# Optimization experiments

Hardware: AMD Instinct MI355X
Metric: run time of the kernel (lower is better)

Reference implementation:

```python
import jax, jax.numpy as jnp
import numpy as np


def _layernorm(x, g, b, eps=1e-5):
    m = jnp.mean(x, axis=-1, keepdims=True)
    v = jnp.var(x, axis=-1, keepdims=True)
    return (x - m) * jax.lax.rsqrt(v + eps) * g + b


def setup_inputs() -> dict:
    B, S, D, NS = 2, 1024, 1024, 2
    key = jax.random.key(0)
    ks = jax.random.split(key, 20)
    w = lambda k, shape: (jax.random.normal(k, shape, dtype=jnp.float32) * 0.02)
    return {
        "id_x": jax.random.normal(ks[0], (B, S, D), dtype=jnp.float32),
        "side": jax.random.normal(ks[1], (B, S, NS, D), dtype=jnp.float32),
        "num_heads": 16,
        "Wq": w(ks[2], (D, D)), "bq": jnp.zeros((D,), jnp.float32),
        "Wk": w(ks[3], (D, D)), "bk": jnp.zeros((D,), jnp.float32),
        "Wv": w(ks[4], (D, D)), "bv": jnp.zeros((D,), jnp.float32),
        "sWq": w(ks[5], (NS, D, D)), "sbq": jnp.zeros((NS, D), jnp.float32),
        "sWk": w(ks[6], (NS, D, D)), "sbk": jnp.zeros((NS, D), jnp.float32),
        "Wo": w(ks[7], (D, D)), "bo": jnp.zeros((D,), jnp.float32),
        "W1": w(ks[8], (D, D)), "b1": jnp.zeros((D,), jnp.float32),
        "W2": w(ks[9], (D, D)), "b2": jnp.zeros((D,), jnp.float32),
        "g1": jnp.ones((D,), jnp.float32), "be1": jnp.zeros((D,), jnp.float32),
        "g2": jnp.ones((D,), jnp.float32), "be2": jnp.zeros((D,), jnp.float32),
    }


def reference(id_x, side, num_heads, Wq, bq, Wk, bk, Wv, bv, sWq, sbq, sWk, sbk,
              Wo, bo, W1, b1, W2, b2, g1, be1, g2, be2):
    B, S, D = id_x.shape
    NS = side.shape[2]
    H = int(num_heads)
    dh = D // H
    scale = 1.0 / np.sqrt(D)  # source scales by sqrt(dim_H), not sqrt(head_dim)

    # id branch QKV: (B,S,H,dh)
    q = (id_x @ Wq + bq).reshape(B, S, H, dh)
    k = (id_x @ Wk + bk).reshape(B, S, H, dh)
    v = (id_x @ Wv + bv).reshape(B, S, H, dh)
    A_id = jax.nn.softmax(jnp.einsum('bqhd,bkhd->bhqk', q, k) * scale, axis=-1)

    # side branches: per-side Q/K projections, (B,S,NS,H,dh)
    sq = (jnp.einsum('bsnd,nde->bsne', side, sWq) + sbq).reshape(B, S, NS, H, dh)
    sk = (jnp.einsum('bsnd,nde->bsne', side, sWk) + sbk).reshape(B, S, NS, H, dh)
    A_side = jax.nn.softmax(
        jnp.einsum('bqnhd,bknhd->bnhqk', sq, sk) * scale, axis=-1)

    # fuse branches via elementwise max over (1+NS) attention maps
    A = jnp.max(jnp.concatenate([A_id[:, None], A_side], axis=1), axis=1)  # (B,H,q,k)

    O = jnp.einsum('bhqk,bkhd->bqhd', A, v).reshape(B, S, D)
    x = id_x + (O @ Wo + bo)          # residual + fc_o
    x = _layernorm(x, g1, be1)        # ln_mha (post-LN)

    # FF block with exact-erf gelu and residual
    h = jax.nn.gelu(x @ W1 + b1, approximate=False)
    x = x + (h @ W2 + b2)
    x = _layernorm(x, g2, be2)        # ln_ff
    return x
```

## Files before the change

### kernel.cpp

```cpp
#include <hip/hip_runtime.h>
#include <hip/hip_bf16.h>
#include <stdint.h>

typedef float   f32x4  __attribute__((ext_vector_type(4)));
typedef __bf16  bf16x8 __attribute__((ext_vector_type(8)));
typedef unsigned short u16x4 __attribute__((ext_vector_type(4)));
typedef unsigned short u16x8 __attribute__((ext_vector_type(8)));

__device__ __forceinline__ uint16_t f2b(float x) {
  union { float f; uint32_t u; } c; c.f = x;
  uint32_t u = c.u;
  return (uint16_t)((u + 0x7FFFu + ((u >> 16) & 1u)) >> 16);
}
__device__ __forceinline__ float b2f(uint16_t x) {
  union { uint32_t u; float f; } c; c.u = ((uint32_t)x) << 16;
  return c.f;
}

__device__ __forceinline__ f32x4 mfma32(bf16x8 a, bf16x8 b, f32x4 c) {
  return __builtin_amdgcn_mfma_f32_16x16x32_bf16(a, b, c, 0, 0, 0);
}

#define GLDS16(g, l) __builtin_amdgcn_global_load_lds( \
    (const __attribute__((address_space(1))) void*)(const void*)(g), \
    (__attribute__((address_space(3))) void*)(void*)(l), 16, 0, 0)

#define WAITVM(N) asm volatile("s_waitcnt vmcnt(" #N ")" ::: "memory")
#define WAITLGKM0 asm volatile("s_waitcnt lgkmcnt(0)" ::: "memory")
#define BAR() __builtin_amdgcn_s_barrier()

__global__ __launch_bounds__(256) void wtrans_all(
    const float* __restrict__ W0, const float* __restrict__ W1,
    const float* __restrict__ W2, const float* __restrict__ W3,
    const float* __restrict__ W4, const float* __restrict__ W5,
    const float* __restrict__ W6, const float* __restrict__ W7,
    const float* __restrict__ W8, const float* __restrict__ W9,
    uint16_t* __restrict__ WT,
    const float* __restrict__ bq, const float* __restrict__ bk,
    const float* __restrict__ bv, const float* __restrict__ sbq,
    const float* __restrict__ sbk, float* __restrict__ biasc,
    const float* __restrict__ id_x, const float* __restrict__ side,
    uint16_t* __restrict__ xb, uint16_t* __restrict__ sdb) {
  __shared__ float tl[32][33];
  const int tx = threadIdx.x, ty = threadIdx.y;
  if (blockIdx.z >= 11) {
    size_t zi = blockIdx.z - 11;
    size_t base = ((zi * 1024 + blockIdx.y * 32 + blockIdx.x) * 256
                   + ty * 32 + tx) * 4;
    const float* in; uint16_t* out;
    if (base < 2097152) { in = id_x; out = xb; }
    else { in = side; out = sdb; base -= 2097152; }
    f32x4 v = *(const f32x4*)(in + base);
    u16x4 o;
    o[0] = f2b(v[0]); o[1] = f2b(v[1]); o[2] = f2b(v[2]); o[3] = f2b(v[3]);
    *(u16x4*)(out + base) = o;
    return;
  }
  if (blockIdx.z == 10) {
    int i = (blockIdx.y * 32 + blockIdx.x) * 256 + ty * 32 + tx;
    if (i < 7168) {
      int seg = i >> 10, off = i & 1023;
      float v;
      switch (seg) {
        case 0: v = bq[off]; break;
        case 1: v = bk[off]; break;
        case 2: v = bv[off]; break;
        case 3: v = sbq[off]; break;
        case 4: v = sbk[off]; break;
        case 5: v = sbq[1024 + off]; break;
        default: v = sbk[1024 + off]; break;
      }
      biasc[i] = v;
    }
    return;
  }
  const float* W;
  switch (blockIdx.z) {
    case 0: W = W0; break; case 1: W = W1; break; case 2: W = W2; break;
    case 3: W = W3; break; case 4: W = W4; break; case 5: W = W5; break;
    case 6: W = W6; break; case 7: W = W7; break; case 8: W = W8; break;
    default: W = W9; break;
  }
  uint16_t* dst = WT + (size_t)blockIdx.z * 1048576;
  const int n0 = blockIdx.x * 32, k0 = blockIdx.y * 32;
#pragma unroll
  for (int i = 0; i < 32; i += 8)
    tl[ty + i][tx] = W[(size_t)(k0 + ty + i) * 1024 + n0 + tx];
  __syncthreads();
#pragma unroll
  for (int i = 0; i < 32; i += 8)
    dst[(size_t)(n0 + ty + i) * 1024 + k0 + tx] = f2b(tl[tx][ty + i]);
}

__global__ __launch_bounds__(512) void proj_k(
    const uint16_t* __restrict__ xb, const uint16_t* __restrict__ sdb,
    const uint16_t* __restrict__ WT, const float* __restrict__ biasc,
    uint16_t* __restrict__ qkv, uint16_t* __restrict__ sqk0,
    uint16_t* __restrict__ sqk1, uint16_t* __restrict__ vT) {
  __shared__ uint16_t As[2][8192];
  __shared__ uint16_t Bs[2][8192];
  const int xcd = blockIdx.x & 7, s = blockIdx.x >> 3;
  const uint16_t* A; const uint16_t* BT; const float* bias; uint16_t* C;
  int lda, ldc, bx, by;
  bool dovt = false;
  if (s < 48) {
    bx = xcd * 3 + s % 3; by = s / 3;
    A = xb; lda = 1024; BT = WT; bias = biasc; C = qkv; ldc = 3072;
    dovt = bx >= 16;
  } else if (s < 80) {
    int r = s - 48; bx = xcd * 2 + (r & 1); by = r >> 1;
    A = sdb; lda = 2048; BT = WT + 3145728; bias = biasc + 3072;
    C = sqk0; ldc = 2048;
  } else {
    int r = s - 80; bx = xcd * 2 + (r & 1); by = r >> 1;
    A = sdb + 1024; lda = 2048; BT = WT + 5242880; bias = biasc + 5120;
    C = sqk1; ldc = 2048;
  }
  const int t = threadIdx.x;
  const int lane = t & 63, w = t >> 6;
  const int wr = w >> 1, wc = w & 1;
  const int l15 = lane & 15, g = lane >> 4;
  const int bm0 = by * 128, bn0 = bx * 128;

  const int scol = ((t & 3) ^ ((t >> 3) & 3)) * 8;
  const uint16_t* ga = A  + (size_t)(bm0 + (t >> 2)) * lda  + scol;
  const uint16_t* gb = BT + (size_t)(bn0 + (t >> 2)) * 1024 + scol;
  const int gsw = (g ^ ((l15 >> 1) & 3)) * 8;

#define GSTAGE(bufi, k0) do { \
    GLDS16(ga + (k0),      &As[bufi][t * 8]); \
    GLDS16(ga + (k0) + 32, &As[bufi][4096 + t * 8]); \
    GLDS16(gb + (k0),      &Bs[bufi][t * 8]); \
    GLDS16(gb + (k0) + 32, &Bs[bufi][4096 + t * 8]); } while (0)

  f32x4 acc[2][4] = {};
  GSTAGE(0, 0);
  int cur = 0;
  for (int it = 0; it < 16; it++) {
    if (it < 15) { GSTAGE(cur ^ 1, (it + 1) * 64); WAITVM(4); }
    else WAITVM(0);
    BAR();
#pragma unroll
    for (int hf = 0; hf < 2; hf++) {
      const int ho = hf * 4096;
      bf16x8 af[2], bf[4];
#pragma unroll
      for (int i = 0; i < 2; i++)
        af[i] = *(const bf16x8*)&As[cur][ho + (wr * 32 + i * 16 + l15) * 32 + gsw];
#pragma unroll
      for (int i = 0; i < 4; i++)
        bf[i] = *(const bf16x8*)&Bs[cur][ho + (wc * 64 + i * 16 + l15) * 32 + gsw];
#pragma unroll
      for (int mi = 0; mi < 2; mi++)
#pragma unroll
        for (int ni = 0; ni < 4; ni++)
          acc[mi][ni] = mfma32(af[mi], bf[ni], acc[mi][ni]);
    }
    WAITLGKM0;
    BAR();
    cur ^= 1;
  }
#undef GSTAGE

#pragma unroll
  for (int mi = 0; mi < 2; mi++) {
#pragma unroll
    for (int ni = 0; ni < 4; ni++) {
      const int row0 = bm0 + wr * 32 + mi * 16 + g * 4;
      const int col  = bn0 + wc * 64 + ni * 16 + l15;
      const float bc = bias[col];
      u16x4 ov;
#pragma unroll
      for (int r = 0; r < 4; r++) {
        float v = acc[mi][ni][r] + bc;
        ov[r] = f2b(v);
        C[(size_t)(row0 + r) * ldc + col] = ov[r];
      }
      if (dovt) {
        const int cc = col - 2048, hh = cc >> 6, dd = cc & 63;
        const int bb = row0 >> 10, s0 = row0 & 1023;
        *(u16x4*)&vT[((size_t)((bb * 16 + hh) * 64 + dd)) * 1024 + s0] = ov;
      }
    }
  }
}

enum { EPI_BF16 = 0, EPI_RES = 1, EPI_GELU = 2 };

template<int EPI>
__global__ __launch_bounds__(256) void gemm64_k(
    const uint16_t* __restrict__ A, int lda,
    const uint16_t* __restrict__ BT,
    const float* __restrict__ bias,
    const float* __restrict__ res,
    void* __restrict__ Cv, int ldc) {
  __shared__ uint16_t As[4][4096];
  __shared__ uint16_t Bs[4][4096];
  const int t = threadIdx.x;
  const int lane = t & 63, w = t >> 6;
  const int wr = w >> 1, wc = w & 1;
  const int l15 = lane & 15, g = lane >> 4;
  const int bm0 = blockIdx.y * 64, bn0 = blockIdx.x * 64;

  const int scol = ((t & 3) ^ ((t >> 3) & 3)) * 8;
  const uint16_t* ga = A  + (size_t)(bm0 + (t >> 2)) * lda  + scol;
  const uint16_t* gb = BT + (size_t)(bn0 + (t >> 2)) * 1024 + scol;
  const int gsw = (g ^ ((l15 >> 1) & 3)) * 8;

#define GSTAGE64(bufi, k0) do { \
    GLDS16(ga + (k0),      &As[bufi][t * 8]); \
    GLDS16(ga + (k0) + 32, &As[bufi][2048 + t * 8]); \
    GLDS16(gb + (k0),      &Bs[bufi][t * 8]); \
    GLDS16(gb + (k0) + 32, &Bs[bufi][2048 + t * 8]); } while (0)

  f32x4 acc[2][2] = {};
  GSTAGE64(0, 0);
  GSTAGE64(1, 64);
  int cur = 0;
  for (int it = 0; it < 16; it++) {
    if (it < 14) {
      GSTAGE64((cur + 2) & 3, (it + 2) * 64);
      WAITVM(8);
    } else if (it == 14) {
      WAITVM(4);
    } else {
      WAITVM(0);
    }
    BAR();
#pragma unroll
    for (int hf = 0; hf < 2; hf++) {
      const int ho = hf * 2048;
      bf16x8 af[2], bf[2];
#pragma unroll
      for (int i = 0; i < 2; i++)
        af[i] = *(const bf16x8*)&As[cur][ho + (wr * 32 + i * 16 + l15) * 32 + gsw];
#pragma unroll
      for (int i = 0; i < 2; i++)
        bf[i] = *(const bf16x8*)&Bs[cur][ho + (wc * 32 + i * 16 + l15) * 32 + gsw];
#pragma unroll
      for (int mi = 0; mi < 2; mi++)
#pragma unroll
        for (int ni = 0; ni < 2; ni++)
          acc[mi][ni] = mfma32(af[mi], bf[ni], acc[mi][ni]);
    }
    cur = (cur + 1) & 3;
  }
#undef GSTAGE64

#pragma unroll
  for (int mi = 0; mi < 2; mi++) {
#pragma unroll
    for (int ni = 0; ni < 2; ni++) {
      const int row0 = bm0 + wr * 32 + mi * 16 + g * 4;
      const int col  = bn0 + wc * 32 + ni * 16 + l15;
      const float bc = bias[col];
#pragma unroll
      for (int r = 0; r < 4; r++) {
        float v = acc[mi][ni][r] + bc;
        const size_t idx = (size_t)(row0 + r) * ldc + col;
        if constexpr (EPI == EPI_RES) {
          ((float*)Cv)[idx] = v + res[idx];
        } else if constexpr (EPI == EPI_GELU) {
          float gl = 0.5f * v * (1.0f + erff(v * 0.70710678118654752f));
          ((uint16_t*)Cv)[idx] = f2b(gl);
        } else {
          ((uint16_t*)Cv)[idx] = f2b(v);
        }
      }
    }
  }
}

__global__ __launch_bounds__(256) void attn_z(
    const uint16_t* __restrict__ qkv,
    const uint16_t* __restrict__ sqk0,
    const uint16_t* __restrict__ sqk1,
    float* __restrict__ zp) {
  __shared__ uint16_t Ks0[3][2048];
  __shared__ uint16_t Ks1[3][2048];
  __shared__ uint16_t Ks2[3][2048];
  const int t = threadIdx.x;
  const int lane = t & 63, w = t >> 6;
  const int l15 = lane & 15, g = lane >> 4;
  const int bid = blockIdx.x;
  const int xcd = bid & 7, idx = bid >> 3;
  const int grp = xcd * 8 + (idx >> 4);
  const int qt = idx & 15;
  const int hb = grp >> 1, kc = grp & 1;
  const int b = hb >> 4, h = hb & 15;
  const int q0 = qt * 64 + w * 16;
  const float scl2 = 0.03125f * 1.44269504088896f;
  const size_t rq = (size_t)(b * 1024 + q0 + l15);

  bf16x8 qf[3][2];
  {
    const uint16_t* p = qkv + rq * 3072 + h * 64 + g * 8;
    qf[0][0] = *(const bf16x8*)p; qf[0][1] = *(const bf16x8*)(p + 32);
    p = sqk0 + rq * 2048 + h * 64 + g * 8;
    qf[1][0] = *(const bf16x8*)p; qf[1][1] = *(const bf16x8*)(p + 32);
    p = sqk1 + rq * 2048 + h * 64 + g * 8;
    qf[2][0] = *(const bf16x8*)p; qf[2][1] = *(const bf16x8*)(p + 32);
  }

  const int p_   = t & 15;
  const int gg_  = (t >> 4) & 3;
  const int hf_  = (t >> 6) & 1;
  const int stq_ = t >> 7;
  const int srow   = (p_ >> 2) * 8 + stq_ * 4 + (p_ & 3) + kc * 512;
  const int kcolel = hf_ * 32 + gg_ * 8;

  const uint16_t* pk0 = qkv  + (size_t)b * 1024 * 3072 + 1024 + h * 64
                      + (size_t)srow * 3072 + kcolel;
  const uint16_t* pk1 = sqk0 + (size_t)b * 1024 * 2048 + 1024 + h * 64
                      + (size_t)srow * 2048 + kcolel;
  const uint16_t* pk2 = sqk1 + (size_t)b * 1024 * 2048 + 1024 + h * 64
                      + (size_t)srow * 2048 + kcolel;

#define STAGE3(bufi) do { \
    GLDS16(pk0, &Ks0[bufi][t * 8]); \
    GLDS16(pk1, &Ks1[bufi][t * 8]); \
    GLDS16(pk2, &Ks2[bufi][t * 8]); \
    pk0 += 32 * 3072; pk1 += 32 * 2048; pk2 += 32 * 2048; } while (0)

  float z0 = 0.f, z1 = 0.f, z2 = 0.f;
  STAGE3(0);
  STAGE3(1);
  int cur = 0;
  for (int kt = 0; kt < 16; kt++) {
    if (kt < 14) {
      int pre = cur + 2; if (pre >= 3) pre -= 3;
      STAGE3(pre);
      WAITVM(6);
    } else if (kt == 14) {
      WAITVM(3);
    } else {
      WAITVM(0);
    }
    BAR();
#pragma unroll
    for (int st = 0; st < 2; st++) {
      f32x4 c0 = {}, c1 = {}, c2 = {};
      c0 = mfma32(*(const bf16x8*)&Ks0[cur][st * 1024 + lane * 8],       qf[0][0], c0);
      c0 = mfma32(*(const bf16x8*)&Ks0[cur][st * 1024 + 512 + lane * 8], qf[0][1], c0);
      c1 = mfma32(*(const bf16x8*)&Ks1[cur][st * 1024 + lane * 8],       qf[1][0], c1);
      c1 = mfma32(*(const bf16x8*)&Ks1[cur][st * 1024 + 512 + lane * 8], qf[1][1], c1);
      c2 = mfma32(*(const bf16x8*)&Ks2[cur][st * 1024 + lane * 8],       qf[2][0], c2);
      c2 = mfma32(*(const bf16x8*)&Ks2[cur][st * 1024 + 512 + lane * 8], qf[2][1], c2);
#pragma unroll
      for (int r = 0; r < 4; r++) {
        z0 += __builtin_amdgcn_exp2f(c0[r] * scl2);
        z1 += __builtin_amdgcn_exp2f(c1[r] * scl2);
        z2 += __builtin_amdgcn_exp2f(c2[r] * scl2);
      }
    }
    WAITLGKM0;
    BAR();
    cur = (cur + 1 == 3) ? 0 : cur + 1;
  }
#undef STAGE3
  z0 += __shfl_xor(z0, 16, 64); z0 += __shfl_xor(z0, 32, 64);
  z1 += __shfl_xor(z1, 16, 64); z1 += __shfl_xor(z1, 32, 64);
  z2 += __shfl_xor(z2, 16, 64); z2 += __shfl_xor(z2, 32, 64);
  if (lane < 16) {
    const int qi = hb * 1024 + q0 + l15;
    zp[kc * 32768 + qi]          = z0;
    zp[65536 + kc * 32768 + qi]  = z1;
    zp[131072 + kc * 32768 + qi] = z2;
  }
}

__global__ __launch_bounds__(256) void attn_o(
    const uint16_t* __restrict__ qkv,
    const uint16_t* __restrict__ sqk0,
    const uint16_t* __restrict__ sqk1,
    const uint16_t* __restrict__ vT,
    const float* __restrict__ zp,
    uint16_t* __restrict__ op) {
  __shared__ uint16_t Ks0[2][2048];
  __shared__ uint16_t Ks1[2][2048];
  __shared__ uint16_t Ks2[2][2048];
  __shared__ uint16_t Vs[2][2048];
  const int t = threadIdx.x;
  const int lane = t & 63, w = t >> 6;
  const int l15 = lane & 15, g = lane >> 4;
  const int bid = blockIdx.x;
  const int xcd = bid & 7, idx = bid >> 3;
  const int grp = xcd * 8 + (idx >> 4);
  const int qt = idx & 15;
  const int hb = grp >> 1, kc = grp & 1;
  const int b = hb >> 4, h = hb & 15;
  const int q0 = qt * 64 + w * 16;
  const float scl2 = 0.03125f * 1.44269504088896f;
  const size_t rq = (size_t)(b * 1024 + q0 + l15);

  bf16x8 qf[3][2];
  {
    const uint16_t* p = qkv + rq * 3072 + h * 64 + g * 8;
    qf[0][0] = *(const bf16x8*)p; qf[0][1] = *(const bf16x8*)(p + 32);
    p = sqk0 + rq * 2048 + h * 64 + g * 8;
    qf[1][0] = *(const bf16x8*)p; qf[1][1] = *(const bf16x8*)(p + 32);
    p = sqk1 + rq * 2048 + h * 64 + g * 8;
    qf[2][0] = *(const bf16x8*)p; qf[2][1] = *(const bf16x8*)(p + 32);
  }
  const int qi = hb * 1024 + q0 + l15;
  const float lz0 = __builtin_amdgcn_logf(zp[qi] + zp[qi + 32768]);
  const float lz1 = __builtin_amdgcn_logf(zp[qi + 65536] + zp[qi + 98304]);
  const float lz2 = __builtin_amdgcn_logf(zp[qi + 131072] + zp[qi + 163840]);

  const int p_   = t & 15;
  const int gg_  = (t >> 4) & 3;
  const int hf_  = (t >> 6) & 1;
  const int stq_ = t >> 7;
  const int srow   = (p_ >> 2) * 8 + stq_ * 4 + (p_ & 3) + kc * 512;
  const int kcolel = hf_ * 32 + gg_ * 8;

  const uint16_t* pk0 = qkv  + (size_t)b * 1024 * 3072 + 1024 + h * 64
                      + (size_t)srow * 3072 + kcolel;
  const uint16_t* pk1 = sqk0 + (size_t)b * 1024 * 2048 + 1024 + h * 64
                      + (size_t)srow * 2048 + kcolel;
  const uint16_t* pk2 = sqk1 + (size_t)b * 1024 * 2048 + 1024 + h * 64
                      + (size_t)srow * 2048 + kcolel;
  const uint16_t* pv  = vT + ((size_t)hb * 64 + (t >> 6) * 16 + p_) * 1024
                      + kc * 512 + gg_ * 8;

#define STAGE4(bufi) do { \
    GLDS16(pk0, &Ks0[bufi][t * 8]); \
    GLDS16(pk1, &Ks1[bufi][t * 8]); \
    GLDS16(pk2, &Ks2[bufi][t * 8]); \
    GLDS16(pv,  &Vs[bufi][t * 8]); \
    pk0 += 32 * 3072; pk1 += 32 * 2048; pk2 += 32 * 2048; pv += 32; } while (0)

  f32x4 accO[4] = {};
  int cur = 0;
  STAGE4(0);
  for (int kt = 0; kt < 16; kt++) {
    if (kt < 15) { STAGE4(cur ^ 1); WAITVM(4); }
    else WAITVM(0);
    BAR();
    u16x8 pu;
#pragma unroll
    for (int sub = 0; sub < 2; sub++) {
      f32x4 c0 = {}, c1 = {}, c2 = {};
      c0 = mfma32(*(const bf16x8*)&Ks0[cur][sub * 1024 + lane * 8],       qf[0][0], c0);
      c0 = mfma32(*(const bf16x8*)&Ks0[cur][sub * 1024 + 512 + lane * 8], qf[0][1], c0);
      c1 = mfma32(*(const bf16x8*)&Ks1[cur][sub * 1024 + lane * 8],       qf[1][0], c1);
      c1 = mfma32(*(const bf16x8*)&Ks1[cur][sub * 1024 + 512 + lane * 8], qf[1][1], c1);
      c2 = mfma32(*(const bf16x8*)&Ks2[cur][sub * 1024 + lane * 8],       qf[2][0], c2);
      c2 = mfma32(*(const bf16x8*)&Ks2[cur][sub * 1024 + 512 + lane * 8], qf[2][1], c2);
#pragma unroll
      for (int r = 0; r < 4; r++) {
        float m = fmaxf(fmaxf(c0[r] * scl2 - lz0, c1[r] * scl2 - lz1),
                        c2[r] * scl2 - lz2);
        pu[sub * 4 + r] = f2b(__builtin_amdgcn_exp2f(m));
      }
    }
    const bf16x8 pf = __builtin_bit_cast(bf16x8, pu);
#pragma unroll
    for (int dt = 0; dt < 4; dt++) {
      bf16x8 vf = *(const bf16x8*)&Vs[cur][dt * 512 + lane * 8];
      accO[dt] = mfma32(vf, pf, accO[dt]);
    }
    WAITLGKM0;
    BAR();
    cur ^= 1;
  }
#undef STAGE4

  uint16_t* ob = op + (size_t)kc * 2097152 + rq * 1024 + h * 64;
#pragma unroll
  for (int dt = 0; dt < 4; dt++) {
    u16x4 o4;
#pragma unroll
    for (int r = 0; r < 4; r++) o4[r] = f2b(accO[dt][r]);
    *(u16x4*)(ob + dt * 16 + g * 4) = o4;
  }
}

__global__ __launch_bounds__(256) void ored_k(const uint16_t* __restrict__ op0,
                                              const uint16_t* __restrict__ op1,
                                              uint16_t* __restrict__ Ob) {
  int i = (blockIdx.x * 256 + threadIdx.x) * 4;
  u16x4 a = *(const u16x4*)(op0 + i);
  u16x4 b = *(const u16x4*)(op1 + i);
  u16x4 o;
#pragma unroll
  for (int j = 0; j < 4; j++) o[j] = f2b(b2f(a[j]) + b2f(b[j]));
  *(u16x4*)(Ob + i) = o;
}

template<int WB>
__global__ __launch_bounds__(256) void ln_k(const float* __restrict__ X,
                                            const float* __restrict__ G,
                                            const float* __restrict__ Bt,
                                            float* __restrict__ Yf,
                                            uint16_t* __restrict__ Yb) {
  const int row = blockIdx.x, t = threadIdx.x;
  const int lane = t & 63, w = t >> 6;
  const size_t base = (size_t)row * 1024 + t * 4;
  f32x4 x = *(const f32x4*)(X + base);
  float s  = x[0] + x[1] + x[2] + x[3];
  float s2 = x[0] * x[0] + x[1] * x[1] + x[2] * x[2] + x[3] * x[3];
#pragma unroll
  for (int o = 1; o < 64; o <<= 1) {
    s  += __shfl_xor(s,  o, 64);
    s2 += __shfl_xor(s2, o, 64);
  }
  __shared__ float red[8];
  if (lane == 0) { red[w] = s; red[4 + w] = s2; }
  __syncthreads();
  s  = red[0] + red[1] + red[2] + red[3];
  s2 = red[4] + red[5] + red[6] + red[7];
  const float mean = s * (1.0f / 1024.0f);
  const float rstd = rsqrtf(s2 * (1.0f / 1024.0f) - mean * mean + 1e-5f);
  f32x4 gv = *(const f32x4*)(G + t * 4);
  f32x4 bv = *(const f32x4*)(Bt + t * 4);
  f32x4 y;
#pragma unroll
  for (int i = 0; i < 4; i++) y[i] = (x[i] - mean) * rstd * gv[i] + bv[i];
  *(f32x4*)(Yf + base) = y;
  if constexpr (WB) {
    u16x4 o;
#pragma unroll
    for (int i = 0; i < 4; i++) o[i] = f2b(y[i]);
    *(u16x4*)(Yb + base) = o;
  }
}

extern "C" void kernel_launch(void* const* d_in, const int* in_sizes, int n_in,
                              void* d_out, int out_size, void* d_ws, size_t ws_size,
                              hipStream_t stream) {
  (void)in_sizes; (void)n_in; (void)out_size;
  const float* id_x = (const float*)d_in[0];
  const float* side = (const float*)d_in[1];
  const float* Wq  = (const float*)d_in[3];
  const float* bq  = (const float*)d_in[4];
  const float* Wk  = (const float*)d_in[5];
  const float* bk  = (const float*)d_in[6];
  const float* Wv  = (const float*)d_in[7];
  const float* bv  = (const float*)d_in[8];
  const float* sWq = (const float*)d_in[9];
  const float* sbq = (const float*)d_in[10];
  const float* sWk = (const float*)d_in[11];
  const float* sbk = (const float*)d_in[12];
  const float* Wo  = (const float*)d_in[13];
  const float* bo  = (const float*)d_in[14];
  const float* W1  = (const float*)d_in[15];
  const float* b1  = (const float*)d_in[16];
  const float* W2  = (const float*)d_in[17];
  const float* b2  = (const float*)d_in[18];
  const float* g1  = (const float*)d_in[19];
  const float* be1 = (const float*)d_in[20];
  const float* g2  = (const float*)d_in[21];
  const float* be2 = (const float*)d_in[22];

  char* ws = (char*)d_ws;
  const size_t oWT   = 0;
  const size_t oBias = 20971520;
  const size_t oZP   = 21000192;
  const size_t oC    = 22179840;
  const size_t oD    = 26374144;
  const size_t oE    = 34762752;
  const size_t total = oE + 33554432;
  if (ws_size < total) return;

  uint16_t* WT    = (uint16_t*)(ws + oWT);
  float*    biasc = (float*)(ws + oBias);
  float*    zp    = (float*)(ws + oZP);
  uint16_t* xb    = (uint16_t*)(ws + oC);
  uint16_t* op0   = (uint16_t*)(ws + oC);
  uint16_t* sdb   = (uint16_t*)(ws + oD);
  uint16_t* Ob    = (uint16_t*)(ws + oD + 4194304);
  char* E = ws + oE;
  uint16_t* qkv  = (uint16_t*)(E);
  uint16_t* sqk0 = (uint16_t*)(E + 12582912);
  uint16_t* sqk1 = (uint16_t*)(E + 20971520);
  uint16_t* vTp  = (uint16_t*)(E + 29360128);
  float*    x1   = (float*)(E);
  float*    x1n  = (float*)(E + 8388608);
  uint16_t* x1nb = (uint16_t*)(E + 16777216);
  uint16_t* hb   = (uint16_t*)(E + 20971520);
  float*    x2   = (float*)(E + 25165824);

  wtrans_all<<<dim3(32, 32, 17), dim3(32, 8), 0, stream>>>(
      Wq, Wk, Wv, sWq, sWk, sWq + 1048576, sWk + 1048576, Wo, W1, W2, WT,
      bq, bk, bv, sbq, sbk, biasc, id_x, side, xb, sdb);

  proj_k<<<896, 512, 0, stream>>>(xb, sdb, WT, biasc, qkv, sqk0, sqk1, vTp);

  attn_z<<<1024, 256, 0, stream>>>(qkv, sqk0, sqk1, zp);
  attn_o<<<1024, 256, 0, stream>>>(qkv, sqk0, sqk1, vTp, zp, op0);
  ored_k<<<2048, 256, 0, stream>>>(op0, op0 + 2097152, Ob);

  gemm64_k<EPI_RES><<<dim3(16, 32), 256, 0, stream>>>(Ob, 1024, WT + 7340032, bo, id_x, x1, 1024);
  ln_k<1><<<2048, 256, 0, stream>>>(x1, g1, be1, x1n, x1nb);
  gemm64_k<EPI_GELU><<<dim3(16, 32), 256, 0, stream>>>(x1nb, 1024, WT + 8388608, b1, nullptr, hb, 1024);
  gemm64_k<EPI_RES><<<dim3(16, 32), 256, 0, stream>>>(hb, 1024, WT + 9437184, b2, x1n, x2, 1024);
  ln_k<0><<<2048, 256, 0, stream>>>(x2, g2, be2, (float*)d_out, nullptr);
}
```

Measured before the change: 181.2 us.

## Double query tile per attention block so K/V tiles are shared across 8 waves

Both attention kernels now launch 512-thread blocks covering 128 query rows instead of 64, halving the grid. Each K and V tile staged in LDS is reused by twice as many waves, and the global-to-LDS loads are split between the two thread halves. attn_z also drops from triple to double buffering. The aim is to cut redundant K/V global traffic per query; the cost is a shallower prefetch pipeline, fewer blocks for latency hiding, and an uneven load split in attn_z.

After: 159.7 us. -11.9%, faster.

```diff
diff --git a/kernel.cpp b/kernel.cpp
--- a/kernel.cpp
+++ b/kernel.cpp
@@ -271,24 +271,23 @@
   }
 }
 
-__global__ __launch_bounds__(256) void attn_z(
+__global__ __launch_bounds__(512) void attn_z(
     const uint16_t* __restrict__ qkv,
     const uint16_t* __restrict__ sqk0,
     const uint16_t* __restrict__ sqk1,
     float* __restrict__ zp) {
-  __shared__ uint16_t Ks0[3][2048];
-  __shared__ uint16_t Ks1[3][2048];
-  __shared__ uint16_t Ks2[3][2048];
+  __shared__ uint16_t Sh[2][6144];
   const int t = threadIdx.x;
   const int lane = t & 63, w = t >> 6;
   const int l15 = lane & 15, g = lane >> 4;
+  const int half = t >> 8, th = t & 255;
   const int bid = blockIdx.x;
   const int xcd = bid & 7, idx = bid >> 3;
-  const int grp = xcd * 8 + (idx >> 4);
-  const int qt = idx & 15;
+  const int grp = xcd * 8 + (idx >> 3);
+  const int qt = idx & 7;
   const int hb = grp >> 1, kc = grp & 1;
   const int b = hb >> 4, h = hb & 15;
-  const int q0 = qt * 64 + w * 16;
+  const int q0 = qt * 128 + w * 16;
   const float scl2 = 0.03125f * 1.44269504088896f;
   const size_t rq = (size_t)(b * 1024 + q0 + l15);
 
@@ -302,50 +301,45 @@
     qf[2][0] = *(const bf16x8*)p; qf[2][1] = *(const bf16x8*)(p + 32);
   }
 
-  const int p_   = t & 15;
-  const int gg_  = (t >> 4) & 3;
-  const int hf_  = (t >> 6) & 1;
-  const int stq_ = t >> 7;
+  const int p_   = th & 15;
+  const int gg_  = (th >> 4) & 3;
+  const int hf_  = (th >> 6) & 1;
+  const int stq_ = th >> 7;
   const int srow   = (p_ >> 2) * 8 + stq_ * 4 + (p_ & 3) + kc * 512;
   const int kcolel = hf_ * 32 + gg_ * 8;
 
-  const uint16_t* pk0 = qkv  + (size_t)b * 1024 * 3072 + 1024 + h * 64
-                      + (size_t)srow * 3072 + kcolel;
-  const uint16_t* pk1 = sqk0 + (size_t)b * 1024 * 2048 + 1024 + h * 64
-                      + (size_t)srow * 2048 + kcolel;
-  const uint16_t* pk2 = sqk1 + (size_t)b * 1024 * 2048 + 1024 + h * 64
-                      + (size_t)srow * 2048 + kcolel;
-
-#define STAGE3(bufi) do { \
-    GLDS16(pk0, &Ks0[bufi][t * 8]); \
-    GLDS16(pk1, &Ks1[bufi][t * 8]); \
-    GLDS16(pk2, &Ks2[bufi][t * 8]); \
-    pk0 += 32 * 3072; pk1 += 32 * 2048; pk2 += 32 * 2048; } while (0)
+  const uint16_t* srcA = half
+      ? sqk0 + (size_t)b * 1024 * 2048 + 1024 + h * 64 + (size_t)srow * 2048 + kcolel
+      : qkv  + (size_t)b * 1024 * 3072 + 1024 + h * 64 + (size_t)srow * 3072 + kcolel;
+  const size_t incA = half ? (size_t)32 * 2048 : (size_t)32 * 3072;
+  const uint16_t* srcB = sqk1 + (size_t)b * 1024 * 2048 + 1024 + h * 64
+                       + (size_t)srow * 2048 + kcolel;
+  const int offA = half * 2048 + th * 8;
+  const int offB = 4096 + th * 8;
+
+#define STAGEZ(bufi) do { \
+    GLDS16(srcA, &Sh[bufi][offA]); \
+    if (!half) GLDS16(srcB, &Sh[bufi][offB]); \
+    srcA += incA; srcB += 32 * 2048; } while (0)
 
   float z0 = 0.f, z1 = 0.f, z2 = 0.f;
-  STAGE3(0);
-  STAGE3(1);
+  STAGEZ(0);
   int cur = 0;
   for (int kt = 0; kt < 16; kt++) {
-    if (kt < 14) {
-      int pre = cur + 2; if (pre >= 3) pre -= 3;
-      STAGE3(pre);
-      WAITVM(6);
-    } else if (kt == 14) {
-      WAITVM(3);
-    } else {
-      WAITVM(0);
-    }
+    if (kt < 15) {
+      STAGEZ(cur ^ 1);
+      if (!half) WAITVM(2); else WAITVM(1);
+    } else WAITVM(0);
     BAR();
 #pragma unroll
     for (int st = 0; st < 2; st++) {
       f32x4 c0 = {}, c1 = {}, c2 = {};
-      c0 = mfma32(*(const bf16x8*)&Ks0[cur][st * 1024 + lane * 8],       qf[0][0], c0);
-      c0 = mfma32(*(const bf16x8*)&Ks0[cur][st * 1024 + 512 + lane * 8], qf[0][1], c0);
-      c1 = mfma32(*(const bf16x8*)&Ks1[cur][st * 1024 + lane * 8],       qf[1][0], c1);
-      c1 = mfma32(*(const bf16x8*)&Ks1[cur][st * 1024 + 512 + lane * 8], qf[1][1], c1);
-      c2 = mfma32(*(const bf16x8*)&Ks2[cur][st * 1024 + lane * 8],       qf[2][0], c2);
-      c2 = mfma32(*(const bf16x8*)&Ks2[cur][st * 1024 + 512 + lane * 8], qf[2][1], c2);
+      c0 = mfma32(*(const bf16x8*)&Sh[cur][st * 1024 + lane * 8],              qf[0][0], c0);
+      c0 = mfma32(*(const bf16x8*)&Sh[cur][st * 1024 + 512 + lane * 8],        qf[0][1], c0);
+      c1 = mfma32(*(const bf16x8*)&Sh[cur][2048 + st * 1024 + lane * 8],       qf[1][0], c1);
+      c1 = mfma32(*(const bf16x8*)&Sh[cur][2048 + st * 1024 + 512 + lane * 8], qf[1][1], c1);
+      c2 = mfma32(*(const bf16x8*)&Sh[cur][4096 + st * 1024 + lane * 8],       qf[2][0], c2);
+      c2 = mfma32(*(const bf16x8*)&Sh[cur][4096 + st * 1024 + 512 + lane * 8], qf[2][1], c2);
 #pragma unroll
       for (int r = 0; r < 4; r++) {
         z0 += __builtin_amdgcn_exp2f(c0[r] * scl2);
@@ -355,9 +349,9 @@
     }
     WAITLGKM0;
     BAR();
-    cur = (cur + 1 == 3) ? 0 : cur + 1;
-  }
-#undef STAGE3
+    cur ^= 1;
+  }
+#undef STAGEZ
   z0 += __shfl_xor(z0, 16, 64); z0 += __shfl_xor(z0, 32, 64);
   z1 += __shfl_xor(z1, 16, 64); z1 += __shfl_xor(z1, 32, 64);
   z2 += __shfl_xor(z2, 16, 64); z2 += __shfl_xor(z2, 32, 64);
@@ -369,27 +363,25 @@
   }
 }
 
-__global__ __launch_bounds__(256) void attn_o(
+__global__ __launch_bounds__(512) void attn_o(
     const uint16_t* __restrict__ qkv,
     const uint16_t* __restrict__ sqk0,
     const uint16_t* __restrict__ sqk1,
     const uint16_t* __restrict__ vT,
     const float* __restrict__ zp,
     uint16_t* __restrict__ op) {
-  __shared__ uint16_t Ks0[2][2048];
-  __shared__ uint16_t Ks1[2][2048];
-  __shared__ uint16_t Ks2[2][2048];
-  __shared__ uint16_t Vs[2][2048];
+  __shared__ uint16_t Sh[2][8192];
   const int t = threadIdx.x;
   const int lane = t & 63, w = t >> 6;
   const int l15 = lane & 15, g = lane >> 4;
+  const int half = t >> 8, th = t & 255;
   const int bid = blockIdx.x;
   const int xcd = bid & 7, idx = bid >> 3;
-  const int grp = xcd * 8 + (idx >> 4);
-  const int qt = idx & 15;
+  const int grp = xcd * 8 + (idx >> 3);
+  const int qt = idx & 7;
   const int hb = grp >> 1, kc = grp & 1;
   const int b = hb >> 4, h = hb & 15;
-  const int q0 = qt * 64 + w * 16;
+  const int q0 = qt * 128 + w * 16;
   const float scl2 = 0.03125f * 1.44269504088896f;
   const size_t rq = (size_t)(b * 1024 + q0 + l15);
 
@@ -407,46 +399,46 @@
   const float lz1 = __builtin_amdgcn_logf(zp[qi + 65536] + zp[qi + 98304]);
   const float lz2 = __builtin_amdgcn_logf(zp[qi + 131072] + zp[qi + 163840]);
 
-  const int p_   = t & 15;
-  const int gg_  = (t >> 4) & 3;
-  const int hf_  = (t >> 6) & 1;
-  const int stq_ = t >> 7;
+  const int p_   = th & 15;
+  const int gg_  = (th >> 4) & 3;
+  const int hf_  = (th >> 6) & 1;
+  const int stq_ = th >> 7;
   const int srow   = (p_ >> 2) * 8 + stq_ * 4 + (p_ & 3) + kc * 512;
   const int kcolel = hf_ * 32 + gg_ * 8;
 
-  const uint16_t* pk0 = qkv  + (size_t)b * 1024 * 3072 + 1024 + h * 64
-                      + (size_t)srow * 3072 + kcolel;
-  const uint16_t* pk1 = sqk0 + (size_t)b * 1024 * 2048 + 1024 + h * 64
-                      + (size_t)srow * 2048 + kcolel;
-  const uint16_t* pk2 = sqk1 + (size_t)b * 1024 * 2048 + 1024 + h * 64
-                      + (size_t)srow * 2048 + kcolel;
-  const uint16_t* pv  = vT + ((size_t)hb * 64 + (t >> 6) * 16 + p_) * 1024
-                      + kc * 512 + gg_ * 8;
-
-#define STAGE4(bufi) do { \
-    GLDS16(pk0, &Ks0[bufi][t * 8]); \
-    GLDS16(pk1, &Ks1[bufi][t * 8]); \
-    GLDS16(pk2, &Ks2[bufi][t * 8]); \
-    GLDS16(pv,  &Vs[bufi][t * 8]); \
-    pk0 += 32 * 3072; pk1 += 32 * 2048; pk2 += 32 * 2048; pv += 32; } while (0)
+  const uint16_t* srcA = half
+      ? sqk0 + (size_t)b * 1024 * 2048 + 1024 + h * 64 + (size_t)srow * 2048 + kcolel
+      : qkv  + (size_t)b * 1024 * 3072 + 1024 + h * 64 + (size_t)srow * 3072 + kcolel;
+  const size_t incA = half ? (size_t)32 * 2048 : (size_t)32 * 3072;
+  const uint16_t* srcB = half
+      ? vT + ((size_t)hb * 64 + (th >> 6) * 16 + p_) * 1024 + kc * 512 + gg_ * 8
+      : sqk1 + (size_t)b * 1024 * 2048 + 1024 + h * 64 + (size_t)srow * 2048 + kcolel;
+  const size_t incB = half ? (size_t)32 : (size_t)32 * 2048;
+  const int offA = half * 2048 + th * 8;
+  const int offB = 4096 + half * 2048 + th * 8;
+
+#define STAGEO(bufi) do { \
+    GLDS16(srcA, &Sh[bufi][offA]); \
+    GLDS16(srcB, &Sh[bufi][offB]); \
+    srcA += incA; srcB += incB; } while (0)
 
   f32x4 accO[4] = {};
+  STAGEO(0);
   int cur = 0;
-  STAGE4(0);
   for (int kt = 0; kt < 16; kt++) {
-    if (kt < 15) { STAGE4(cur ^ 1); WAITVM(4); }
+    if (kt < 15) { STAGEO(cur ^ 1); WAITVM(2); }
     else WAITVM(0);
     BAR();
     u16x8 pu;
 #pragma unroll
     for (int sub = 0; sub < 2; sub++) {
       f32x4 c0 = {}, c1 = {}, c2 = {};
-      c0 = mfma32(*(const bf16x8*)&Ks0[cur][sub * 1024 + lane * 8],       qf[0][0], c0);
-      c0 = mfma32(*(const bf16x8*)&Ks0[cur][sub * 1024 + 512 + lane * 8], qf[0][1], c0);
-      c1 = mfma32(*(const bf16x8*)&Ks1[cur][sub * 1024 + lane * 8],       qf[1][0], c1);
-      c1 = mfma32(*(const bf16x8*)&Ks1[cur][sub * 1024 + 512 + lane * 8], qf[1][1], c1);
-      c2 = mfma32(*(const bf16x8*)&Ks2[cur][sub * 1024 + lane * 8],       qf[2][0], c2);
-      c2 = mfma32(*(const bf16x8*)&Ks2[cur][sub * 1024 + 512 + lane * 8], qf[2][1], c2);
+      c0 = mfma32(*(const bf16x8*)&Sh[cur][sub * 1024 + lane * 8],              qf[0][0], c0);
+      c0 = mfma32(*(const bf16x8*)&Sh[cur][sub * 1024 + 512 + lane * 8],        qf[0][1], c0);
+      c1 = mfma32(*(const bf16x8*)&Sh[cur][2048 + sub * 1024 + lane * 8],       qf[1][0], c1);
+      c1 = mfma32(*(const bf16x8*)&Sh[cur][2048 + sub * 1024 + 512 + lane * 8], qf[1][1], c1);
+      c2 = mfma32(*(const bf16x8*)&Sh[cur][4096 + sub * 1024 + lane * 8],       qf[2][0], c2);
+      c2 = mfma32(*(const bf16x8*)&Sh[cur][4096 + sub * 1024 + 512 + lane * 8], qf[2][1], c2);
 #pragma unroll
       for (int r = 0; r < 4; r++) {
         float m = fmaxf(fmaxf(c0[r] * scl2 - lz0, c1[r] * scl2 - lz1),
@@ -457,14 +449,14 @@
     const bf16x8 pf = __builtin_bit_cast(bf16x8, pu);
 #pragma unroll
     for (int dt = 0; dt < 4; dt++) {
-      bf16x8 vf = *(const bf16x8*)&Vs[cur][dt * 512 + lane * 8];
+      bf16x8 vf = *(const bf16x8*)&Sh[cur][6144 + dt * 512 + lane * 8];
       accO[dt] = mfma32(vf, pf, accO[dt]);
     }
     WAITLGKM0;
     BAR();
     cur ^= 1;
   }
-#undef STAGE4
+#undef STAGEO
 
   uint16_t* ob = op + (size_t)kc * 2097152 + rq * 1024 + h * 64;
 #pragma unroll
@@ -587,8 +579,8 @@
 
   proj_k<<<896, 512, 0, stream>>>(xb, sdb, WT, biasc, qkv, sqk0, sqk1, vTp);
 
-  attn_z<<<1024, 256, 0, stream>>>(qkv, sqk0, sqk1, zp);
-  attn_o<<<1024, 256, 0, stream>>>(qkv, sqk0, sqk1, vTp, zp, op0);
+  attn_z<<<512, 512, 0, stream>>>(qkv, sqk0, sqk1, zp);
+  attn_o<<<512, 512, 0, stream>>>(qkv, sqk0, sqk1, vTp, zp, op0);
   ored_k<<<2048, 256, 0, stream>>>(op0, op0 + 2097152, Ob);
 
   gemm64_k<EPI_RES><<<dim3(16, 32), 256, 0, stream>>>(Ob, 1024, WT + 7340032, bo, id_x, x1, 1024);
```
